# Kernel tuning notes

Measured on AMD Instinct MI355X. Metric: run time of the kernel, lower is better.

## Reference

```python
import jax, jax.numpy as jnp
import numpy as np

HEAD_SIZE = 64
N_EMBED = 1024
THETA = 10000.0


def _rope_cos_sin(T, dim):
    # freqs = 1/theta^(2i/dim), i in [0, dim//2)
    freqs = 1.0 / (THETA ** (jnp.arange(0, dim, 2, dtype=jnp.float32) / dim))  # (dim//2,)
    angles = jnp.arange(T, dtype=jnp.float32)[:, None] * freqs[None, :]        # (T, dim//2)
    return jnp.cos(angles), jnp.sin(angles)


def _apply_rope(q, cos, sin):
    # q: (B, T, hs); interpret consecutive pairs as complex (even=real, odd=imag)
    B, T, hs = q.shape
    qr = q.reshape(B, T, hs // 2, 2)
    ev, od = qr[..., 0], qr[..., 1]
    out_ev = ev * cos - od * sin
    out_od = ev * sin + od * cos
    return jnp.stack([out_ev, out_od], axis=-1).reshape(B, T, hs)


def setup_inputs() -> dict:
    key = jax.random.key(0)
    ks = jax.random.split(key, 7)
    B, T = 4, 2048
    s = 1.0 / np.sqrt(N_EMBED)
    return {
        "x": jax.random.normal(ks[0], (B, T, N_EMBED), dtype=jnp.float32),
        "mask": jnp.ones((B, T), dtype=jnp.int32),
        "Wq": jax.random.uniform(ks[1], (N_EMBED, HEAD_SIZE), jnp.float32, -s, s),
        "bq": jax.random.uniform(ks[2], (HEAD_SIZE,), jnp.float32, -s, s),
        "Wk": jax.random.uniform(ks[3], (N_EMBED, HEAD_SIZE), jnp.float32, -s, s),
        "bk": jax.random.uniform(ks[4], (HEAD_SIZE,), jnp.float32, -s, s),
        "Wv": jax.random.uniform(ks[5], (N_EMBED, HEAD_SIZE), jnp.float32, -s, s),
        "bv": jax.random.uniform(ks[6], (HEAD_SIZE,), jnp.float32, -s, s),
    }


def reference(x, mask, Wq, bq, Wk, bk, Wv, bv):
    B, T, C = x.shape
    Q = x @ Wq + bq  # (B, T, hs)
    K = x @ Wk + bk
    V = x @ Wv + bv

    cos, sin = _rope_cos_sin(T, HEAD_SIZE)
    Q = _apply_rope(Q, cos, sin)
    K = _apply_rope(K, cos, sin)

    causal = jnp.triu(jnp.ones((T, T), dtype=bool), k=1)[None, :, :]  # (1, T, T)
    pad = (mask == 0)[:, :, None]                                     # (B, T, 1) masks rows
    attn_mask = causal | pad                                          # (B, T, T)

    scores = jnp.einsum('btd,bsd->bts', Q, K) * (C ** -0.5)
    scores = jnp.where(attn_mask, -jnp.inf, scores)
    attn = jax.nn.softmax(scores, axis=-1)
    # dropout in eval mode: identity
    return jnp.einsum('bts,bsd->btd', attn, V)
```

## Files before the change

### kernel.cpp

```cpp
#include <hip/hip_runtime.h>
#include <math.h>


typedef __attribute__((ext_vector_type(8))) short short8v;
typedef __attribute__((ext_vector_type(4))) float f32x4;

__device__ __forceinline__ unsigned short f2bf(float f){
  unsigned int u = __float_as_uint(f);
  u += 0x7fffu + ((u >> 16) & 1u);
  return (unsigned short)(u >> 16);
}
__device__ __forceinline__ float bf2f(unsigned short h){
  return __uint_as_float(((unsigned int)h) << 16);
}
__device__ __forceinline__ f32x4 mfma16(short8v a, short8v b, f32x4 c){
  return __builtin_amdgcn_mfma_f32_16x16x32_bf16(a, b, c, 0, 0, 0);
}


__global__ __launch_bounds__(256) void prep_k(
    const float* __restrict__ Wq, const float* __restrict__ Wk, const float* __restrict__ Wv,
    unsigned short* __restrict__ WThi, unsigned short* __restrict__ WTlo,
    float2* __restrict__ rope)
{
  __shared__ __align__(16) unsigned short Th[64][72], Tl[64][72];
  const int t  = threadIdx.x;
  const int k0 = blockIdx.x * 64;
  const int mtx = blockIdx.y;
  const float* Wsrc = (mtx == 0) ? Wq : (mtx == 1 ? Wk : Wv);
  const int n0 = mtx * 64;

  {
    const int r  = t >> 2;
    const int cb = (t & 3) * 16;
    #pragma unroll
    for (int j4 = 0; j4 < 4; ++j4){
      const float4 v4 = *(const float4*)&Wsrc[(k0 + r) * 64 + cb + j4 * 4];
      const float f[4] = {v4.x, v4.y, v4.z, v4.w};
      #pragma unroll
      for (int u = 0; u < 4; ++u){
        const unsigned short hi = f2bf(f[u]);
        Th[cb + j4*4 + u][r] = hi;
        Tl[cb + j4*4 + u][r] = f2bf(f[u] - bf2f(hi));
      }
    }
  }
  __syncthreads();
  {
    const int n  = t >> 2;
    const int kc = (t & 3) * 16;
    #pragma unroll
    for (int c = 0; c < 2; ++c){
      *(short8v*)&WThi[(size_t)(n0 + n) * 1024 + k0 + kc + c*8] = *(const short8v*)&Th[n][kc + c*8];
      *(short8v*)&WTlo[(size_t)(n0 + n) * 1024 + k0 + kc + c*8] = *(const short8v*)&Tl[n][kc + c*8];
    }
  }
  const int gtid = (blockIdx.y * 16 + blockIdx.x) * 256 + t;
  for (int idx = gtid; idx < 65536; idx += 48 * 256){
    const int p = idx & 31, tt = idx >> 5;
    const float freq = exp2f((float)p * -0.4152410118609203f);
    float s, c;
    sincosf((float)tt * freq, &s, &c);
    rope[idx] = make_float2(c, s);
  }
}

__global__ __launch_bounds__(512) void qkv_k(
    const float* __restrict__ x,
    const unsigned short* __restrict__ WThi, const unsigned short* __restrict__ WTlo,
    const float* __restrict__ bq, const float* __restrict__ bk, const float* __restrict__ bv,
    const float2* __restrict__ rope,
    unsigned short* __restrict__ Qb, unsigned short* __restrict__ Kb,
    unsigned short* __restrict__ VT)
{
  __shared__ __align__(16) unsigned short XAh[64][72], XAl[64][72];
  __shared__ __align__(16) unsigned short WTh[96][72], WTl[96][72];

  const int t = threadIdx.x;
  const int w = t >> 6, l = t & 63;
  const int rg = w & 3, cg = w >> 2;
  const int g = l >> 4, c16 = l & 15;
  const int m0 = blockIdx.x * 64;
  const int n0 = blockIdx.y * 96;

  f32x4 acc[3];
  #pragma unroll
  for (int nt = 0; nt < 3; ++nt) acc[nt] = (f32x4){0.f, 0.f, 0.f, 0.f};

  const int xr = t >> 3, xc = (t & 7) * 8;

  for (int k0 = 0; k0 < 1024; k0 += 64){
    __syncthreads();
    {
      const float* xp = &x[(size_t)(m0 + xr) * 1024 + k0 + xc];
      const float4 a4 = *(const float4*)xp;
      const float4 b4 = *(const float4*)(xp + 4);
      const float f[8] = {a4.x, a4.y, a4.z, a4.w, b4.x, b4.y, b4.z, b4.w};
      union { short8v v; unsigned short u[8]; } hh, ll;
      #pragma unroll
      for (int j = 0; j < 8; ++j){
        hh.u[j] = f2bf(f[j]);
        ll.u[j] = f2bf(f[j] - bf2f(hh.u[j]));
      }
      *(short8v*)&XAh[xr][xc] = hh.v;
      *(short8v*)&XAl[xr][xc] = ll.v;
    }
    #pragma unroll
    for (int a = 0; a < 3; ++a){
      const int ch = t + 512 * a;
      const int cc = (ch < 768) ? ch : ch - 768;
      const int wn = cc >> 3, wk = (cc & 7) * 8;
      const size_t go = (size_t)(n0 + wn) * 1024 + k0 + wk;
      if (ch < 768) *(short8v*)&WTh[wn][wk] = *(const short8v*)&WThi[go];
      else          *(short8v*)&WTl[wn][wk] = *(const short8v*)&WTlo[go];
    }
    __syncthreads();
    #pragma unroll
    for (int ks = 0; ks < 2; ++ks){
      const short8v ah  = *(const short8v*)&XAh[16*rg + c16][ks*32 + g*8];
      const short8v al2 = *(const short8v*)&XAl[16*rg + c16][ks*32 + g*8];
      #pragma unroll
      for (int nt = 0; nt < 3; ++nt){
        const int wr = 48*cg + 16*nt + c16;
        const short8v bh = *(const short8v*)&WTh[wr][ks*32 + g*8];
        const short8v bl = *(const short8v*)&WTl[wr][ks*32 + g*8];
        acc[nt] = mfma16(ah, bh, acc[nt]);
        acc[nt] = mfma16(ah, bl, acc[nt]);
        acc[nt] = mfma16(al2, bh, acc[nt]);
      }
    }
  }

  #pragma unroll
  for (int nt = 0; nt < 3; ++nt){
    const int c = n0 + 48*cg + 16*nt + c16;
    const int m = c >> 6, cm = c & 63;
    const float* bptr = (m == 0) ? bq : (m == 1 ? bk : bv);
    const float bias = bptr[cm];
    #pragma unroll
    for (int i = 0; i < 4; ++i){
      const int gr = m0 + 16*rg + 4*g + i;
      float v = acc[nt][i] + bias;
      const float other = __shfl_xor(v, 1);
      if (m < 2){
        const float2 cs = rope[(gr & 2047) * 32 + (cm >> 1)];
        v = (c & 1) ? fmaf(v, cs.x,  other * cs.y)
                    : fmaf(v, cs.x, -other * cs.y);
      }
      if (m == 0)      Qb[(size_t)gr*64 + cm] = f2bf(v);
      else if (m == 1) Kb[(size_t)gr*64 + cm] = f2bf(v);
      else             VT[((size_t)(gr >> 11) * 64 + cm) * 2048 + (gr & 2047)] = f2bf(v);
    }
  }
}

__global__ __launch_bounds__(1024) void attn_k(
    const unsigned short* __restrict__ Qb, const unsigned short* __restrict__ Kb,
    const unsigned short* __restrict__ VT, float* __restrict__ out)
{
  __shared__ __align__(16) unsigned short Ph[16][16][24];
  __shared__ float Om[2][7][16][68];
  __shared__ float Ml[2][7][16][2];

  const int t = threadIdx.x;
  const int w = t >> 6, l = t & 63;
  const int h = w & 1, kh = w >> 1;
  const int g = l >> 4, c16 = l & 15;
  const int b = blockIdx.y;
  const int q0 = (63 - (int)blockIdx.x) * 32;
  const size_t bT = (size_t)b * 2048;

  short8v qh0, qh1;
  {
    const size_t qoff = (bT + q0 + 16*h + c16) * 64 + g*8;
    qh0 = *(const short8v*)&Qb[qoff];
    qh1 = *(const short8v*)&Qb[qoff + 32];
  }

  const unsigned short* Kbase = &Kb[(bT + 16*kh + c16) * 64 + g*8];
  const unsigned short* Vbase = &VT[((size_t)b*64 + c16) * 2048 + 16*kh + 8*(g & 1)];

  f32x4 acc[4];
  #pragma unroll
  for (int nt = 0; nt < 4; ++nt) acc[nt] = (f32x4){0.f, 0.f, 0.f, 0.f};
  float m_run[4], l_run[4];
  #pragma unroll
  for (int i = 0; i < 4; ++i){ m_run[i] = -INFINITY; l_run[i] = 0.f; }

  const int nk = q0 / 128 + 1;
  const short8v zero8 = (short8v){0,0,0,0,0,0,0,0};

  short8v kb0c = *(const short8v*)&Kbase[0];
  short8v kb1c = *(const short8v*)&Kbase[32];

  for (int kt = 0; kt < nk; ++kt){
    const int k0 = kt * 128;
    short8v vb0 = zero8, vb1 = zero8, vb2 = zero8, vb3 = zero8;
    if (g < 2){
      vb0 = *(const short8v*)&Vbase[k0];
      vb1 = *(const short8v*)&Vbase[k0 + 32768];
      vb2 = *(const short8v*)&Vbase[k0 + 65536];
      vb3 = *(const short8v*)&Vbase[k0 + 98304];
    }
    const int kn = (kt + 1 < nk ? kt + 1 : kt) * 128;
    const short8v kb0n = *(const short8v*)&Kbase[(size_t)kn * 64];
    const short8v kb1n = *(const short8v*)&Kbase[(size_t)kn * 64 + 32];

    f32x4 z = (f32x4){0.f, 0.f, 0.f, 0.f};
    z = mfma16(qh0, kb0c, z);
    z = mfma16(qh1, kb1c, z);

    float sv[4];
    #pragma unroll
    for (int i = 0; i < 4; ++i){
      float v = z[i] * 0.03125f;
      if (kt == nk - 1){
        const int keyg = k0 + 16*kh + c16;
        const int qg = q0 + 16*h + 4*g + i;
        if (keyg > qg) v = -INFINITY;
      }
      sv[i] = v;
    }

    float al[4];
    #pragma unroll
    for (int i = 0; i < 4; ++i){
      float pm = sv[i];
      pm = fmaxf(pm, __shfl_xor(pm, 1));
      pm = fmaxf(pm, __shfl_xor(pm, 2));
      pm = fmaxf(pm, __shfl_xor(pm, 4));
      pm = fmaxf(pm, __shfl_xor(pm, 8));
      const float mnew = fmaxf(m_run[i], pm);
      const float msafe = fmaxf(mnew, -1e30f);
      al[i] = expf(m_run[i] - msafe);
      const float p0 = expf(sv[i] - msafe);
      float ps = p0;
      ps += __shfl_xor(ps, 1);
      ps += __shfl_xor(ps, 2);
      ps += __shfl_xor(ps, 4);
      ps += __shfl_xor(ps, 8);
      l_run[i] = l_run[i] * al[i] + ps;
      m_run[i] = mnew;
      Ph[w][4*g + i][c16] = f2bf(p0);
    }

    #pragma unroll
    for (int nt = 0; nt < 4; ++nt)
      #pragma unroll
      for (int i = 0; i < 4; ++i) acc[nt][i] *= al[i];

    short8v pa = zero8;
    if (g < 2) pa = *(const short8v*)&Ph[w][c16][g*8];
    acc[0] = mfma16(pa, vb0, acc[0]);
    acc[1] = mfma16(pa, vb1, acc[1]);
    acc[2] = mfma16(pa, vb2, acc[2]);
    acc[3] = mfma16(pa, vb3, acc[3]);

    kb0c = kb0n; kb1c = kb1n;
  }

  if (kh > 0){
    #pragma unroll
    for (int nt = 0; nt < 4; ++nt)
      #pragma unroll
      for (int i = 0; i < 4; ++i)
        Om[h][kh-1][4*g + i][16*nt + c16] = acc[nt][i];
    if (c16 == 0){
      #pragma unroll
      for (int i = 0; i < 4; ++i){
        Ml[h][kh-1][4*g + i][0] = m_run[i];
        Ml[h][kh-1][4*g + i][1] = l_run[i];
      }
    }
  }
  __syncthreads();
  if (kh == 0){
    float es[4], e[7][4], linv[4];
    #pragma unroll
    for (int i = 0; i < 4; ++i){
      float mo[7], lo[7];
      float mm = m_run[i];
      #pragma unroll
      for (int j = 0; j < 7; ++j){
        mo[j] = Ml[h][j][4*g + i][0];
        lo[j] = Ml[h][j][4*g + i][1];
        mm = fmaxf(mm, mo[j]);
      }
      es[i] = expf(m_run[i] - mm);
      float lt = l_run[i] * es[i];
      #pragma unroll
      for (int j = 0; j < 7; ++j){
        e[j][i] = (mo[j] == -INFINITY) ? 0.f : expf(mo[j] - mm);
        lt += lo[j] * e[j][i];
      }
      linv[i] = 1.f / lt;
    }
    #pragma unroll
    for (int nt = 0; nt < 4; ++nt)
      #pragma unroll
      for (int i = 0; i < 4; ++i){
        float v = acc[nt][i] * es[i];
        #pragma unroll
        for (int j = 0; j < 7; ++j)
          v += Om[h][j][4*g + i][16*nt + c16] * e[j][i];
        out[(bT + q0 + 16*h + 4*g + i) * 64 + 16*nt + c16] = v * linv[i];
      }
  }
}

extern "C" void kernel_launch(void* const* d_in, const int* in_sizes, int n_in,
                              void* d_out, int out_size, void* d_ws, size_t ws_size,
                              hipStream_t stream) {
  (void)in_sizes; (void)n_in; (void)out_size; (void)ws_size;
  const float* x    = (const float*)d_in[0];
  const float* Wq   = (const float*)d_in[2];
  const float* bq   = (const float*)d_in[3];
  const float* Wk   = (const float*)d_in[4];
  const float* bk   = (const float*)d_in[5];
  const float* Wv   = (const float*)d_in[6];
  const float* bv   = (const float*)d_in[7];
  float* out = (float*)d_out;

  const size_t NROW = 8192;
  unsigned short* Qb   = (unsigned short*)d_ws;
  unsigned short* Kb   = Qb  + NROW * 64;
  unsigned short* VT   = Kb  + NROW * 64;
  unsigned short* WThi = VT  + NROW * 64;
  unsigned short* WTlo = WThi + 192 * 1024;
  float2*         rope = (float2*)(WTlo + 192 * 1024);

  prep_k<<<dim3(16, 3), dim3(256), 0, stream>>>(Wq, Wk, Wv, WThi, WTlo, rope);
  qkv_k<<<dim3(128, 2), dim3(512), 0, stream>>>(x, WThi, WTlo, bq, bk, bv, rope,
                                                Qb, Kb, VT);
  attn_k<<<dim3(64, 4), dim3(1024), 0, stream>>>(Qb, Kb, VT, out);
}
```

Measured before the change: 164.6 us.

## Drop split-bf16 precision in QKV projection and use direct-from-global MFMA tiles

Replaces the three-MFMA hi/lo split-bf16 GEMM for the QKV projection with a single plain bf16 MFMA per tile. It also removes the LDS staging: each wave now loads x and the transposed weights straight from global memory in 16x32 tiles, on a 768-block grid. This cuts MFMA work threefold, removes the lo-weight buffer and its conversion, and eliminates the block barriers. In exchange it loses precision in Q/K/V, and each wave re-reads x rows without any LDS reuse.

```diff
diff --git a/kernel.cpp b/kernel.cpp
--- a/kernel.cpp
+++ b/kernel.cpp
@@ -20,10 +20,9 @@
 
 __global__ __launch_bounds__(256) void prep_k(
     const float* __restrict__ Wq, const float* __restrict__ Wk, const float* __restrict__ Wv,
-    unsigned short* __restrict__ WThi, unsigned short* __restrict__ WTlo,
-    float2* __restrict__ rope)
+    unsigned short* __restrict__ WTb, float2* __restrict__ rope)
 {
-  __shared__ __align__(16) unsigned short Th[64][72], Tl[64][72];
+  __shared__ __align__(16) unsigned short Th[64][72];
   const int t  = threadIdx.x;
   const int k0 = blockIdx.x * 64;
   const int mtx = blockIdx.y;
@@ -36,13 +35,10 @@
     #pragma unroll
     for (int j4 = 0; j4 < 4; ++j4){
       const float4 v4 = *(const float4*)&Wsrc[(k0 + r) * 64 + cb + j4 * 4];
-      const float f[4] = {v4.x, v4.y, v4.z, v4.w};
-      #pragma unroll
-      for (int u = 0; u < 4; ++u){
-        const unsigned short hi = f2bf(f[u]);
-        Th[cb + j4*4 + u][r] = hi;
-        Tl[cb + j4*4 + u][r] = f2bf(f[u] - bf2f(hi));
-      }
+      Th[cb + j4*4 + 0][r] = f2bf(v4.x);
+      Th[cb + j4*4 + 1][r] = f2bf(v4.y);
+      Th[cb + j4*4 + 2][r] = f2bf(v4.z);
+      Th[cb + j4*4 + 3][r] = f2bf(v4.w);
     }
   }
   __syncthreads();
@@ -50,10 +46,8 @@
     const int n  = t >> 2;
     const int kc = (t & 3) * 16;
     #pragma unroll
-    for (int c = 0; c < 2; ++c){
-      *(short8v*)&WThi[(size_t)(n0 + n) * 1024 + k0 + kc + c*8] = *(const short8v*)&Th[n][kc + c*8];
-      *(short8v*)&WTlo[(size_t)(n0 + n) * 1024 + k0 + kc + c*8] = *(const short8v*)&Tl[n][kc + c*8];
-    }
+    for (int c = 0; c < 2; ++c)
+      *(short8v*)&WTb[(size_t)(n0 + n) * 1024 + k0 + kc + c*8] = *(const short8v*)&Th[n][kc + c*8];
   }
   const int gtid = (blockIdx.y * 16 + blockIdx.x) * 256 + t;
   for (int idx = gtid; idx < 65536; idx += 48 * 256){
@@ -65,82 +59,55 @@
   }
 }
 
-__global__ __launch_bounds__(512) void qkv_k(
+__global__ __launch_bounds__(256) void qkv_k(
     const float* __restrict__ x,
-    const unsigned short* __restrict__ WThi, const unsigned short* __restrict__ WTlo,
+    const unsigned short* __restrict__ WTb,
     const float* __restrict__ bq, const float* __restrict__ bk, const float* __restrict__ bv,
     const float2* __restrict__ rope,
     unsigned short* __restrict__ Qb, unsigned short* __restrict__ Kb,
     unsigned short* __restrict__ VT)
 {
-  __shared__ __align__(16) unsigned short XAh[64][72], XAl[64][72];
-  __shared__ __align__(16) unsigned short WTh[96][72], WTl[96][72];
-
   const int t = threadIdx.x;
   const int w = t >> 6, l = t & 63;
-  const int rg = w & 3, cg = w >> 2;
   const int g = l >> 4, c16 = l & 15;
-  const int m0 = blockIdx.x * 64;
-  const int n0 = blockIdx.y * 96;
-
-  f32x4 acc[3];
+  const int mgp = blockIdx.x / 3, ngp = blockIdx.x % 3;
+  const int mg = mgp * 2 + (w >> 1);
+  const int ng = ngp * 2 + (w & 1);
+  const int m0 = mg * 16, n0 = ng * 32;
+
+  const float*          xr  = x   + (size_t)(m0 + c16) * 1024 + g*8;
+  const unsigned short* wr0 = WTb + (size_t)(n0 + c16) * 1024 + g*8;
+  const unsigned short* wr1 = WTb + (size_t)(n0 + 16 + c16) * 1024 + g*8;
+
+  f32x4 acc0 = (f32x4){0.f,0.f,0.f,0.f};
+  f32x4 acc1 = (f32x4){0.f,0.f,0.f,0.f};
+
+  #pragma unroll 4
+  for (int k0 = 0; k0 < 1024; k0 += 32){
+    const float4 a4 = *(const float4*)(xr + k0);
+    const float4 b4 = *(const float4*)(xr + k0 + 4);
+    union { short8v v; unsigned short u[8]; } aa;
+    aa.u[0] = f2bf(a4.x); aa.u[1] = f2bf(a4.y);
+    aa.u[2] = f2bf(a4.z); aa.u[3] = f2bf(a4.w);
+    aa.u[4] = f2bf(b4.x); aa.u[5] = f2bf(b4.y);
+    aa.u[6] = f2bf(b4.z); aa.u[7] = f2bf(b4.w);
+    const short8v wb0 = *(const short8v*)(wr0 + k0);
+    const short8v wb1 = *(const short8v*)(wr1 + k0);
+    acc0 = mfma16(aa.v, wb0, acc0);
+    acc1 = mfma16(aa.v, wb1, acc1);
+  }
+
+  f32x4 accs[2] = {acc0, acc1};
   #pragma unroll
-  for (int nt = 0; nt < 3; ++nt) acc[nt] = (f32x4){0.f, 0.f, 0.f, 0.f};
-
-  const int xr = t >> 3, xc = (t & 7) * 8;
-
-  for (int k0 = 0; k0 < 1024; k0 += 64){
-    __syncthreads();
-    {
-      const float* xp = &x[(size_t)(m0 + xr) * 1024 + k0 + xc];
-      const float4 a4 = *(const float4*)xp;
-      const float4 b4 = *(const float4*)(xp + 4);
-      const float f[8] = {a4.x, a4.y, a4.z, a4.w, b4.x, b4.y, b4.z, b4.w};
-      union { short8v v; unsigned short u[8]; } hh, ll;
-      #pragma unroll
-      for (int j = 0; j < 8; ++j){
-        hh.u[j] = f2bf(f[j]);
-        ll.u[j] = f2bf(f[j] - bf2f(hh.u[j]));
-      }
-      *(short8v*)&XAh[xr][xc] = hh.v;
-      *(short8v*)&XAl[xr][xc] = ll.v;
-    }
-    #pragma unroll
-    for (int a = 0; a < 3; ++a){
-      const int ch = t + 512 * a;
-      const int cc = (ch < 768) ? ch : ch - 768;
-      const int wn = cc >> 3, wk = (cc & 7) * 8;
-      const size_t go = (size_t)(n0 + wn) * 1024 + k0 + wk;
-      if (ch < 768) *(short8v*)&WTh[wn][wk] = *(const short8v*)&WThi[go];
-      else          *(short8v*)&WTl[wn][wk] = *(const short8v*)&WTlo[go];
-    }
-    __syncthreads();
-    #pragma unroll
-    for (int ks = 0; ks < 2; ++ks){
-      const short8v ah  = *(const short8v*)&XAh[16*rg + c16][ks*32 + g*8];
-      const short8v al2 = *(const short8v*)&XAl[16*rg + c16][ks*32 + g*8];
-      #pragma unroll
-      for (int nt = 0; nt < 3; ++nt){
-        const int wr = 48*cg + 16*nt + c16;
-        const short8v bh = *(const short8v*)&WTh[wr][ks*32 + g*8];
-        const short8v bl = *(const short8v*)&WTl[wr][ks*32 + g*8];
-        acc[nt] = mfma16(ah, bh, acc[nt]);
-        acc[nt] = mfma16(ah, bl, acc[nt]);
-        acc[nt] = mfma16(al2, bh, acc[nt]);
-      }
-    }
-  }
-
-  #pragma unroll
-  for (int nt = 0; nt < 3; ++nt){
-    const int c = n0 + 48*cg + 16*nt + c16;
+  for (int nt = 0; nt < 2; ++nt){
+    const int c = n0 + 16*nt + c16;
     const int m = c >> 6, cm = c & 63;
     const float* bptr = (m == 0) ? bq : (m == 1 ? bk : bv);
     const float bias = bptr[cm];
     #pragma unroll
     for (int i = 0; i < 4; ++i){
-      const int gr = m0 + 16*rg + 4*g + i;
-      float v = acc[nt][i] + bias;
+      const int gr = m0 + 4*g + i;
+      float v = accs[nt][i] + bias;
       const float other = __shfl_xor(v, 1);
       if (m < 2){
         const float2 cs = rope[(gr & 2047) * 32 + (cm >> 1)];
@@ -325,12 +292,10 @@
   unsigned short* Qb   = (unsigned short*)d_ws;
   unsigned short* Kb   = Qb  + NROW * 64;
   unsigned short* VT   = Kb  + NROW * 64;
-  unsigned short* WThi = VT  + NROW * 64;
-  unsigned short* WTlo = WThi + 192 * 1024;
-  float2*         rope = (float2*)(WTlo + 192 * 1024);
-
-  prep_k<<<dim3(16, 3), dim3(256), 0, stream>>>(Wq, Wk, Wv, WThi, WTlo, rope);
-  qkv_k<<<dim3(128, 2), dim3(512), 0, stream>>>(x, WThi, WTlo, bq, bk, bv, rope,
-                                                Qb, Kb, VT);
+  unsigned short* WTb  = VT  + NROW * 64;
+  float2*         rope = (float2*)(WTb + 192 * 1024);
+
+  prep_k<<<dim3(16, 3), dim3(256), 0, stream>>>(Wq, Wk, Wv, WTb, rope);
+  qkv_k<<<dim3(768), dim3(256), 0, stream>>>(x, WTb, bq, bk, bv, rope, Qb, Kb, VT);
   attn_k<<<dim3(64, 4), dim3(1024), 0, stream>>>(Qb, Kb, VT, out);
 }
```

New measurement: 167.4 us. No clear change (+1.7%).
